# Kernel optimization log

Measured on AMD Instinct MI355X. Metric: run time of the kernel, lower is better.

Reference implementation:

```python
import jax, jax.numpy as jnp
import numpy as np

N, E = 100000, 1600000
NFEAT, NHID, NCLASS, NLAYER = 128, 128, 40, 3


def _glorot(key, shape):
    fan_in, fan_out = shape[0], shape[1]
    lim = float(np.sqrt(6.0 / (fan_in + fan_out)))
    return jax.random.uniform(key, shape, jnp.float32, -lim, lim)


def setup_inputs() -> dict:
    key = jax.random.key(0)
    ks = jax.random.split(key, 12)
    x = jax.random.normal(ks[0], (N, NFEAT), jnp.float32)
    src = jax.random.randint(ks[1], (E,), 0, N, jnp.int32)
    dst = jax.random.randint(ks[2], (E,), 0, N, jnp.int32)
    W1 = _glorot(ks[3], (NFEAT, NHID)); b1 = jnp.zeros((NHID,), jnp.float32)
    W2 = _glorot(ks[4], (NHID, NHID)); b2 = jnp.zeros((NHID,), jnp.float32)
    Wg = jnp.stack([_glorot(ks[5 + l], (NHID, NHID)) for l in range(NLAYER)])  # [L,H,H]
    bg = jnp.zeros((NLAYER, NHID), jnp.float32)
    Wc = _glorot(ks[5 + NLAYER], (NHID, NCLASS)); bc = jnp.zeros((NCLASS,), jnp.float32)
    return {"x": x, "src": src, "dst": dst, "W1": W1, "b1": b1, "W2": W2,
            "b2": b2, "Wg": Wg, "bg": bg, "Wc": Wc, "bc": bc}


def _graph_conv(h, src, dst, W, b, out_norm, in_norm):
    # DGL GraphConv norm='both': scale by src out-deg^{-1/2}, sum-aggregate,
    # scale by dst in-deg^{-1/2}, then linear (in_feats == out_feats -> W after agg).
    h = h * out_norm[:, None]
    agg = jax.ops.segment_sum(h[src], dst, num_segments=N)
    return (agg * in_norm[:, None]) @ W + b


def reference(x, src, dst, W1, b1, W2, b2, Wg, bg, Wc, bc):
    ones = jnp.ones((E,), jnp.float32)
    out_deg = jnp.clip(jax.ops.segment_sum(ones, src, num_segments=N), 1.0)
    in_deg = jnp.clip(jax.ops.segment_sum(ones, dst, num_segments=N), 1.0)
    out_norm = jax.lax.rsqrt(out_deg)
    in_norm = jax.lax.rsqrt(in_deg)

    h = x @ W1 + b1            # feature1
    h = h @ W2 + b2            # feature2
    for l in range(NLAYER):    # stacked GraphConv + ReLU (dropout is identity in eval)
        h = _graph_conv(h, src, dst, Wg[l], bg[l], out_norm, in_norm)
        h = jax.nn.relu(h)
    return h @ Wc + bc         # classifier
```

## Files before the change

### kernel.cpp

```cpp
#include <hip/hip_runtime.h>
#include <hip/hip_fp16.h>
#include <cstdint>
#include <cstddef>

constexpr int NN  = 100000;
constexpr int EE  = 1600000;
constexpr int HID = 128;
constexpr int BUK = 256;
constexpr int NBUK = (NN + BUK - 1) / BUK;
constexpr int BLKE = 2048;
constexpr int NBE  = (EE + BLKE - 1) / BLKE;
constexpr int MH   = NBUK * NBE;
constexpr int NSC  = (MH + 1023) / 1024;

typedef float f32x4_t __attribute__((ext_vector_type(4)));
typedef short bf16x8_t __attribute__((ext_vector_type(8)));

static __device__ __forceinline__ short f2bf(float f) {
    union { float f; unsigned u; } x; x.f = f;
    unsigned r = x.u + 0x7FFF + ((x.u >> 16) & 1);
    return (short)(r >> 16);
}
static __device__ __forceinline__ float bf2f(short b) {
    union { unsigned u; float f; } x; x.u = ((unsigned)(unsigned short)b) << 16;
    return x.f;
}

__global__ __launch_bounds__(256) void bh_both_k(const int* __restrict__ src, const int* __restrict__ dst,
                                                 int* __restrict__ bh_d, int* __restrict__ bh_s) {
    __shared__ int hd[NBUK], hs[NBUK];
    int blk = blockIdx.x, t = threadIdx.x;
    for (int i = t; i < NBUK; i += 256) { hd[i] = 0; hs[i] = 0; }
    __syncthreads();
    int e0 = blk * BLKE, e1 = min(e0 + BLKE, EE);
    for (int e = e0 + t; e < e1; e += 256) {
        atomicAdd(&hd[dst[e] >> 8], 1);
        atomicAdd(&hs[src[e] >> 8], 1);
    }
    __syncthreads();
    for (int i = t; i < NBUK; i += 256) {
        bh_d[i * NBE + blk] = hd[i];
        bh_s[i * NBE + blk] = hs[i];
    }
}

__global__ __launch_bounds__(256) void scan_sum_k(const int* __restrict__ in, int* __restrict__ bsum, int n) {
    __shared__ int sc[256];
    int b = blockIdx.x, t = threadIdx.x;
    int base = b * 1024 + t * 4;
    int s = 0;
#pragma unroll
    for (int j = 0; j < 4; j++) { int idx = base + j; s += (idx < n) ? in[idx] : 0; }
    sc[t] = s; __syncthreads();
    for (int off = 128; off > 0; off >>= 1) {
        if (t < off) sc[t] += sc[t + off];
        __syncthreads();
    }
    if (t == 0) bsum[b] = sc[0];
}

__global__ __launch_bounds__(512) void scan_top_k(const int* __restrict__ bsum, int* __restrict__ boff, int nb) {
    __shared__ int sc[512];
    int t = threadIdx.x;
    int v = (t < nb) ? bsum[t] : 0;
    sc[t] = v; __syncthreads();
    for (int off = 1; off < 512; off <<= 1) {
        int u = (t >= off) ? sc[t - off] : 0;
        __syncthreads();
        sc[t] += u;
        __syncthreads();
    }
    if (t < nb) boff[t] = sc[t] - v;
}

__global__ __launch_bounds__(256) void scan_chunk_k(const int* __restrict__ in, const int* __restrict__ boff,
                                                    int* __restrict__ out, int n) {
    __shared__ int sc[256];
    int b = blockIdx.x, t = threadIdx.x;
    int base = b * 1024 + t * 4;
    int c[4];
#pragma unroll
    for (int j = 0; j < 4; j++) { int idx = base + j; c[j] = (idx < n) ? in[idx] : 0; }
    int s = c[0] + c[1] + c[2] + c[3];
    sc[t] = s; __syncthreads();
    for (int off = 1; off < 256; off <<= 1) {
        int v = (t >= off) ? sc[t - off] : 0;
        __syncthreads();
        sc[t] += v;
        __syncthreads();
    }
    int excl = sc[t] - s + boff[b];
#pragma unroll
    for (int j = 0; j < 4; j++) {
        int idx = base + j;
        if (idx < n) out[idx] = excl;
        excl += c[j];
    }
}

__global__ __launch_bounds__(256) void scatter_both_k(const int* __restrict__ src, const int* __restrict__ dst,
                                                      const int* __restrict__ off_d, const int* __restrict__ off_s,
                                                      unsigned* __restrict__ pairs, unsigned char* __restrict__ sbyte) {
    __shared__ int cd[NBUK], cs[NBUK];
    int blk = blockIdx.x, t = threadIdx.x;
    for (int i = t; i < NBUK; i += 256) {
        cd[i] = off_d[i * NBE + blk];
        cs[i] = off_s[i * NBE + blk];
    }
    __syncthreads();
    int e0 = blk * BLKE, e1 = min(e0 + BLKE, EE);
    for (int e = e0 + t; e < e1; e += 256) {
        int d = dst[e], s = src[e];
        int pd = atomicAdd(&cd[d >> 8], 1);
        pairs[pd] = ((unsigned)(d & 255) << 17) | (unsigned)s;
        int ps = atomicAdd(&cs[s >> 8], 1);
        sbyte[ps] = (unsigned char)(s & 255);
    }
}

__global__ __launch_bounds__(512) void bucket_csr_ocnt_k(
    const unsigned* __restrict__ pairs, const int* __restrict__ off_d,
    const unsigned char* __restrict__ sbyte, const int* __restrict__ off_s,
    int* __restrict__ rowptr, int* __restrict__ col,
    float* __restrict__ inorm, float* __restrict__ onorm) {
    __shared__ int hist[BUK];
    __shared__ int excl[BUK];
    __shared__ int psum[BUK];
    int t = threadIdx.x;

    if (blockIdx.x >= NBUK) {
        int b = blockIdx.x - NBUK;
        int base = off_s[b * NBE];
        int endv = (b == NBUK - 1) ? EE : off_s[(b + 1) * NBE];
        if (t < BUK) hist[t] = 0;
        __syncthreads();
        for (int i = base + t; i < endv; i += 512) atomicAdd(&hist[sbyte[i]], 1);
        __syncthreads();
        if (t < BUK) {
            int node = b * BUK + t;
            if (node < NN) {
                int c = hist[t]; if (c < 1) c = 1;
                onorm[node] = rsqrtf((float)c);
            }
        }
        return;
    }

    int b = blockIdx.x;
    int base = off_d[b * NBE];
    int endv = (b == NBUK - 1) ? EE : off_d[(b + 1) * NBE];
    if (t < BUK) hist[t] = 0;
    __syncthreads();
    for (int i = base + t; i < endv; i += 512) atomicAdd(&hist[pairs[i] >> 17], 1);
    __syncthreads();
    int ps = 0;
    if (t < BUK) { ps = hist[t]; psum[t] = ps; }
    __syncthreads();
    for (int off = 1; off < BUK; off <<= 1) {
        int u = 0;
        if (t < BUK && t >= off) u = psum[t - off];
        __syncthreads();
        if (t < BUK) psum[t] += u;
        __syncthreads();
    }
    if (t < BUK) {
        int pex = psum[t] - ps;
        excl[t] = pex;
        int node = b * BUK + t;
        if (node < NN) {
            rowptr[node] = base + pex;
            int c = ps; if (c < 1) c = 1;
            inorm[node] = rsqrtf((float)c);
        }
    }
    if (b == NBUK - 1 && t == 0) rowptr[NN] = EE;
    __syncthreads();
    for (int i = base + t; i < endv; i += 512) {
        unsigned p = pairs[i];
        int pos = base + atomicAdd(&excl[p >> 17], 1);
        col[pos] = (int)(p & 0x1FFFFu);
    }
}

__global__ __launch_bounds__(256) void w12_k(const float* __restrict__ W1, const float* __restrict__ W2,
                                             const float* __restrict__ b1, const float* __restrict__ b2,
                                             float* __restrict__ W12, float* __restrict__ b12) {
    if (blockIdx.x == 64) {
        int j = threadIdx.x;
        if (j < 128) {
            float acc = b2[j];
            for (int k = 0; k < 128; k++) acc = fmaf(b1[k], W2[k * 128 + j], acc);
            b12[j] = acc;
        }
        return;
    }
    int idx = blockIdx.x * 256 + threadIdx.x;
    int i = idx >> 7, j = idx & 127;
    float a0 = 0.f, a1 = 0.f, a2 = 0.f, a3 = 0.f;
    for (int k = 0; k < 128; k += 4) {
        a0 = fmaf(W1[i * 128 + k],     W2[(k)     * 128 + j], a0);
        a1 = fmaf(W1[i * 128 + k + 1], W2[(k + 1) * 128 + j], a1);
        a2 = fmaf(W1[i * 128 + k + 2], W2[(k + 2) * 128 + j], a2);
        a3 = fmaf(W1[i * 128 + k + 3], W2[(k + 3) * 128 + j], a3);
    }
    W12[idx] = (a0 + a1) + (a2 + a3);
}

__global__ __launch_bounds__(256) void agg_k(const float4* __restrict__ h16, const int* __restrict__ rowptr,
                                             const int* __restrict__ col, float4* __restrict__ out) {
    int w = (int)((blockIdx.x * 256 + threadIdx.x) >> 6);
    if (w >= NN) return;
    int lane = threadIdx.x & 63;
    int q   = lane >> 4;
    int l16 = lane & 15;
    int beg = rowptr[w], end = rowptr[w + 1];
    float acc[8];
#pragma unroll
    for (int j = 0; j < 8; j++) acc[j] = 0.f;

    union HU { float4 f4; __half2 h2[4]; };
    int i = beg + q;
    for (; i + 12 < end; i += 16) {
        int s0 = col[i], s1 = col[i + 4], s2 = col[i + 8], s3 = col[i + 12];
        HU u0, u1, u2, u3;
        u0.f4 = h16[(size_t)s0 * 16 + l16];
        u1.f4 = h16[(size_t)s1 * 16 + l16];
        u2.f4 = h16[(size_t)s2 * 16 + l16];
        u3.f4 = h16[(size_t)s3 * 16 + l16];
#pragma unroll
        for (int p = 0; p < 4; p++) {
            float2 a = __half22float2(u0.h2[p]);
            float2 b = __half22float2(u1.h2[p]);
            float2 c = __half22float2(u2.h2[p]);
            float2 d = __half22float2(u3.h2[p]);
            acc[2 * p]     += (a.x + b.x) + (c.x + d.x);
            acc[2 * p + 1] += (a.y + b.y) + (c.y + d.y);
        }
    }
    for (; i < end; i += 4) {
        int s = col[i];
        HU u; u.f4 = h16[(size_t)s * 16 + l16];
#pragma unroll
        for (int p = 0; p < 4; p++) {
            float2 a = __half22float2(u.h2[p]);
            acc[2 * p]     += a.x;
            acc[2 * p + 1] += a.y;
        }
    }
#pragma unroll
    for (int mm = 16; mm <= 32; mm <<= 1)
#pragma unroll
        for (int j = 0; j < 8; j++) acc[j] += __shfl_xor(acc[j], mm);
    if (q == 0) {
        float4 o0, o1;
        o0.x = acc[0]; o0.y = acc[1]; o0.z = acc[2]; o0.w = acc[3];
        o1.x = acc[4]; o1.y = acc[5]; o1.z = acc[6]; o1.w = acc[7];
        out[(size_t)w * 32 + l16 * 2]     = o0;
        out[(size_t)w * 32 + l16 * 2 + 1] = o1;
    }
}

template <int NT, bool RELU, bool INSCALE, bool OUTSCALE, bool OUTHALF>
__global__ __launch_bounds__(256) void mfma_gemm_k(
    const float* __restrict__ in, const float* __restrict__ inscale,
    const float* __restrict__ W, const float* __restrict__ bias,
    void* __restrict__ outp, const float* __restrict__ outscale,
    int nrows, int ncols, int ntiles) {

    __shared__ short Bh[NT * 2048];
    __shared__ short Bl[NT * 2048];

    const int t = threadIdx.x;

    if constexpr (NT == 8) {
        for (int j = 0; j < 16; j++) {
            int fi = (j * 256 + t) * 4;
            int k = fi >> 7, n0 = fi & 127;
            float4 wv = *(const float4*)(W + fi);
            float wa[4] = {wv.x, wv.y, wv.z, wv.w};
#pragma unroll
            for (int cc = 0; cc < 4; cc++) {
                int g = n0 + cc;
                int q2 = g >> 2;
                int ntc = q2 & 7;
                int c = ((q2 >> 3) << 2) | (g & 3);
                int kblk = k >> 5, ksub = k & 31;
                int lane_ = ((ksub >> 3) << 4) | c;
                int sidx = ((ntc * 4 + kblk) * 64 + lane_) * 8 + (ksub & 7);
                short hi = f2bf(wa[cc]);
                Bh[sidx] = hi; Bl[sidx] = f2bf(wa[cc] - bf2f(hi));
            }
        }
    } else {
        for (int idx = t; idx < 128 * 64; idx += 256) {
            int k = idx >> 6, g = idx & 63;
            if (g < NT * 16) {
                float w = (g < 40) ? W[k * 40 + g] : 0.f;
                int q2 = g >> 2;
                int ntc = q2 % NT;
                int c = (q2 / NT) * 4 + (g & 3);
                int kblk = k >> 5, ksub = k & 31;
                int lane_ = ((ksub >> 3) << 4) | c;
                int sidx = ((ntc * 4 + kblk) * 64 + lane_) * 8 + (ksub & 7);
                short hi = f2bf(w);
                Bh[sidx] = hi; Bl[sidx] = f2bf(w - bf2f(hi));
            }
        }
    }
    __syncthreads();

    const int wave = t >> 6;
    const int lane = t & 63;
    const int m    = lane & 15;
    const int kq   = lane >> 4;
    const int cbase = kq * 4 * NT;

    float bstat[4 * NT];
#pragma unroll
    for (int i = 0; i < 4 * NT; i++) {
        int g = cbase + i;
        bstat[i] = (g < ncols) ? bias[g] : 0.f;
    }

    const int wstride = gridDim.x * 4;
    for (int tile = blockIdx.x * 4 + wave; tile < ntiles; tile += wstride) {
        int row = tile * 16 + m;
        bool rv = row < nrows;

        bf16x8_t Ah[4], Al[4];
        float s = 1.f;
        if (INSCALE && rv) s = inscale[row];
#pragma unroll
        for (int kb = 0; kb < 4; kb++) {
            const float* ap = in + (size_t)row * 128 + kb * 32 + kq * 8;
            float4 p0, p1;
            if (rv) { p0 = *(const float4*)ap; p1 = *(const float4*)(ap + 4); }
            else    { p0 = make_float4(0,0,0,0); p1 = make_float4(0,0,0,0); }
            float av[8] = {p0.x, p0.y, p0.z, p0.w, p1.x, p1.y, p1.z, p1.w};
#pragma unroll
            for (int j = 0; j < 8; j++) {
                float v = INSCALE ? av[j] * s : av[j];
                short hi = f2bf(v);
                Ah[kb][j] = hi;
                Al[kb][j] = f2bf(v - bf2f(hi));
            }
        }

        float osc = 1.f;
        if (OUTSCALE && rv) osc = outscale[row];

        float ov[4 * NT] __attribute__((aligned(16)));
#pragma unroll
        for (int nt = 0; nt < NT; nt++) {
            f32x4_t acc = {0.f, 0.f, 0.f, 0.f};
#pragma unroll
            for (int kb = 0; kb < 4; kb++) {
                const bf16x8_t bh = *(const bf16x8_t*)&Bh[((nt * 4 + kb) * 64 + lane) * 8];
                const bf16x8_t bl = *(const bf16x8_t*)&Bl[((nt * 4 + kb) * 64 + lane) * 8];
                acc = __builtin_amdgcn_mfma_f32_16x16x32_bf16(bh, Ah[kb], acc, 0, 0, 0);
                acc = __builtin_amdgcn_mfma_f32_16x16x32_bf16(bh, Al[kb], acc, 0, 0, 0);
                acc = __builtin_amdgcn_mfma_f32_16x16x32_bf16(bl, Ah[kb], acc, 0, 0, 0);
            }
#pragma unroll
            for (int r = 0; r < 4; r++) {
                float v = acc[r] + bstat[nt * 4 + r];
                if (RELU) v = fmaxf(v, 0.f);
                ov[nt * 4 + r] = v * osc;
            }
        }

        if (rv) {
            if constexpr (OUTHALF) {
                union { __half h[4 * NT]; float4 f4[NT]; } U;
#pragma unroll
                for (int i = 0; i < 4 * NT; i++) U.h[i] = __float2half_rn(ov[i]);
                float4* p = (float4*)((__half*)outp + (size_t)row * ncols + cbase);
#pragma unroll
                for (int j = 0; j < NT; j += 2) p[j >> 1] = U.f4[j >> 1];
            } else if constexpr (NT == 8) {
                float4* p = (float4*)((float*)outp + (size_t)row * 128 + cbase);
#pragma unroll
                for (int j = 0; j < 8; j++) p[j] = ((const float4*)ov)[j];
            } else {
                float* p = (float*)outp + (size_t)row * 40 + cbase;
#pragma unroll
                for (int j = 0; j < 3; j++) {
                    if (cbase + j * 4 < 40) *(float4*)(p + j * 4) = ((const float4*)ov)[j];
                }
            }
        }
    }
}

extern "C" void kernel_launch(void* const* d_in, const int* in_sizes, int n_in,
                              void* d_out, int out_size, void* d_ws, size_t ws_size,
                              hipStream_t stream) {
    const float* x   = (const float*)d_in[0];
    const int*   src = (const int*)d_in[1];
    const int*   dst = (const int*)d_in[2];
    const float* W1  = (const float*)d_in[3];
    const float* b1  = (const float*)d_in[4];
    const float* W2  = (const float*)d_in[5];
    const float* b2  = (const float*)d_in[6];
    const float* Wg  = (const float*)d_in[7];
    const float* bg  = (const float*)d_in[8];
    const float* Wc  = (const float*)d_in[9];
    const float* bc  = (const float*)d_in[10];
    float* out = (float*)d_out;

    char* ws = (char*)d_ws;
    size_t off = 0;
    auto alloc = [&](size_t bytes) -> void* {
        void* p = ws + off;
        off += (bytes + 255) & ~(size_t)255;
        return p;
    };
    float*  h0     = (float*)alloc((size_t)NN * HID * 4);
    float*  h1     = (float*)alloc((size_t)NN * HID * 4);
    __half* h16    = (__half*)alloc((size_t)NN * HID * 2);
    float*  W12    = (float*)alloc(128 * 128 * 4);
    float*  b12    = (float*)alloc(128 * 4);
    float*  onorm  = (float*)alloc((size_t)NN * 4);
    float*  inorm  = (float*)alloc((size_t)NN * 4);
    int*    rowptr = (int*)alloc((size_t)(NN + 1) * 4);
    int*    col    = (int*)alloc((size_t)EE * 4);
    int*    bh_d   = (int*)alloc((size_t)MH * 4);
    int*    bh_s   = (int*)alloc((size_t)MH * 4);
    int*    off_d  = (int*)alloc((size_t)MH * 4);
    int*    off_s  = (int*)alloc((size_t)MH * 4);
    int*    bsum   = (int*)alloc((size_t)NSC * 4);
    int*    boff   = (int*)alloc((size_t)NSC * 4);
    unsigned*      pairs = (unsigned*)h0;
    unsigned char* sbyte = (unsigned char*)h0 + (size_t)EE * 4;

    bh_both_k<<<NBE, 256, 0, stream>>>(src, dst, bh_d, bh_s);
    scan_sum_k<<<NSC, 256, 0, stream>>>(bh_d, bsum, MH);
    scan_top_k<<<1, 512, 0, stream>>>(bsum, boff, NSC);
    scan_chunk_k<<<NSC, 256, 0, stream>>>(bh_d, boff, off_d, MH);
    scan_sum_k<<<NSC, 256, 0, stream>>>(bh_s, bsum, MH);
    scan_top_k<<<1, 512, 0, stream>>>(bsum, boff, NSC);
    scan_chunk_k<<<NSC, 256, 0, stream>>>(bh_s, boff, off_s, MH);
    scatter_both_k<<<NBE, 256, 0, stream>>>(src, dst, off_d, off_s, pairs, sbyte);
    bucket_csr_ocnt_k<<<2 * NBUK, 512, 0, stream>>>(pairs, off_d, sbyte, off_s,
                                                    rowptr, col, inorm, onorm);

    w12_k<<<65, 256, 0, stream>>>(W1, W2, b1, b2, W12, b12);

    const int ntiles = (NN + 15) / 16;
    const int ggrid  = 512;

    mfma_gemm_k<8, false, false, true, true><<<ggrid, 256, 0, stream>>>(
        x, nullptr, W12, b12, h16, onorm, NN, 128, ntiles);
    for (int l = 0; l < 3; l++) {
        agg_k<<<(NN * 64 + 255) / 256, 256, 0, stream>>>(
            (const float4*)h16, rowptr, col, (float4*)h0);
        if (l < 2) {
            mfma_gemm_k<8, true, true, true, true><<<ggrid, 256, 0, stream>>>(
                h0, inorm, Wg + (size_t)l * 128 * 128, bg + (size_t)l * 128, h16, onorm, NN, 128, ntiles);
        } else {
            mfma_gemm_k<8, true, true, false, false><<<ggrid, 256, 0, stream>>>(
                h0, inorm, Wg + (size_t)l * 128 * 128, bg + (size_t)l * 128, h1, nullptr, NN, 128, ntiles);
        }
    }
    mfma_gemm_k<3, false, false, false, false><<<ggrid, 256, 0, stream>>>(
        h1, nullptr, Wc, bc, out, nullptr, NN, 40, ntiles);
}
```

Baseline: 558.6 us.

## Merge src/dst bucket scans, fold in-norm into aggregation, unroll agg tail

The dst and src bucket histograms now sit in one concatenated array, so a single three-kernel scan replaces two; src offsets are recovered by subtracting the edge count. The in-degree normalisation moves from the GEMM input path into the aggregation epilogue, and the aggregation tail loop handles two neighbours per iteration. This removes three small launches and a per-element scale in the GEMM load, and also changes ntiles to NN/16, which relies on NN being a multiple of 16.

```diff
diff --git a/kernel.cpp b/kernel.cpp
--- a/kernel.cpp
+++ b/kernel.cpp
@@ -11,7 +11,8 @@
 constexpr int BLKE = 2048;
 constexpr int NBE  = (EE + BLKE - 1) / BLKE;
 constexpr int MH   = NBUK * NBE;
-constexpr int NSC  = (MH + 1023) / 1024;
+constexpr int MH2  = 2 * MH;
+constexpr int NSC  = (MH2 + 2047) / 2048;
 
 typedef float f32x4_t __attribute__((ext_vector_type(4)));
 typedef short bf16x8_t __attribute__((ext_vector_type(8)));
@@ -27,7 +28,7 @@
 }
 
 __global__ __launch_bounds__(256) void bh_both_k(const int* __restrict__ src, const int* __restrict__ dst,
-                                                 int* __restrict__ bh_d, int* __restrict__ bh_s) {
+                                                 int* __restrict__ bh2) {
     __shared__ int hd[NBUK], hs[NBUK];
     int blk = blockIdx.x, t = threadIdx.x;
     for (int i = t; i < NBUK; i += 256) { hd[i] = 0; hs[i] = 0; }
@@ -39,18 +40,18 @@
     }
     __syncthreads();
     for (int i = t; i < NBUK; i += 256) {
-        bh_d[i * NBE + blk] = hd[i];
-        bh_s[i * NBE + blk] = hs[i];
+        bh2[i * NBE + blk]      = hd[i];
+        bh2[MH + i * NBE + blk] = hs[i];
     }
 }
 
 __global__ __launch_bounds__(256) void scan_sum_k(const int* __restrict__ in, int* __restrict__ bsum, int n) {
     __shared__ int sc[256];
     int b = blockIdx.x, t = threadIdx.x;
-    int base = b * 1024 + t * 4;
+    int base = b * 2048 + t * 8;
     int s = 0;
 #pragma unroll
-    for (int j = 0; j < 4; j++) { int idx = base + j; s += (idx < n) ? in[idx] : 0; }
+    for (int j = 0; j < 8; j++) { int idx = base + j; s += (idx < n) ? in[idx] : 0; }
     sc[t] = s; __syncthreads();
     for (int off = 128; off > 0; off >>= 1) {
         if (t < off) sc[t] += sc[t + off];
@@ -77,11 +78,11 @@
                                                     int* __restrict__ out, int n) {
     __shared__ int sc[256];
     int b = blockIdx.x, t = threadIdx.x;
-    int base = b * 1024 + t * 4;
-    int c[4];
-#pragma unroll
-    for (int j = 0; j < 4; j++) { int idx = base + j; c[j] = (idx < n) ? in[idx] : 0; }
-    int s = c[0] + c[1] + c[2] + c[3];
+    int base = b * 2048 + t * 8;
+    int c[8];
+    int s = 0;
+#pragma unroll
+    for (int j = 0; j < 8; j++) { int idx = base + j; c[j] = (idx < n) ? in[idx] : 0; s += c[j]; }
     sc[t] = s; __syncthreads();
     for (int off = 1; off < 256; off <<= 1) {
         int v = (t >= off) ? sc[t - off] : 0;
@@ -91,7 +92,7 @@
     }
     int excl = sc[t] - s + boff[b];
 #pragma unroll
-    for (int j = 0; j < 4; j++) {
+    for (int j = 0; j < 8; j++) {
         int idx = base + j;
         if (idx < n) out[idx] = excl;
         excl += c[j];
@@ -99,13 +100,13 @@
 }
 
 __global__ __launch_bounds__(256) void scatter_both_k(const int* __restrict__ src, const int* __restrict__ dst,
-                                                      const int* __restrict__ off_d, const int* __restrict__ off_s,
+                                                      const int* __restrict__ off2,
                                                       unsigned* __restrict__ pairs, unsigned char* __restrict__ sbyte) {
     __shared__ int cd[NBUK], cs[NBUK];
     int blk = blockIdx.x, t = threadIdx.x;
     for (int i = t; i < NBUK; i += 256) {
-        cd[i] = off_d[i * NBE + blk];
-        cs[i] = off_s[i * NBE + blk];
+        cd[i] = off2[i * NBE + blk];
+        cs[i] = off2[MH + i * NBE + blk] - EE;
     }
     __syncthreads();
     int e0 = blk * BLKE, e1 = min(e0 + BLKE, EE);
@@ -119,8 +120,8 @@
 }
 
 __global__ __launch_bounds__(512) void bucket_csr_ocnt_k(
-    const unsigned* __restrict__ pairs, const int* __restrict__ off_d,
-    const unsigned char* __restrict__ sbyte, const int* __restrict__ off_s,
+    const unsigned* __restrict__ pairs, const unsigned char* __restrict__ sbyte,
+    const int* __restrict__ off2,
     int* __restrict__ rowptr, int* __restrict__ col,
     float* __restrict__ inorm, float* __restrict__ onorm) {
     __shared__ int hist[BUK];
@@ -130,8 +131,8 @@
 
     if (blockIdx.x >= NBUK) {
         int b = blockIdx.x - NBUK;
-        int base = off_s[b * NBE];
-        int endv = (b == NBUK - 1) ? EE : off_s[(b + 1) * NBE];
+        int base = off2[MH + b * NBE] - EE;
+        int endv = (b == NBUK - 1) ? EE : off2[MH + (b + 1) * NBE] - EE;
         if (t < BUK) hist[t] = 0;
         __syncthreads();
         for (int i = base + t; i < endv; i += 512) atomicAdd(&hist[sbyte[i]], 1);
@@ -147,8 +148,8 @@
     }
 
     int b = blockIdx.x;
-    int base = off_d[b * NBE];
-    int endv = (b == NBUK - 1) ? EE : off_d[(b + 1) * NBE];
+    int base = off2[b * NBE];
+    int endv = (b == NBUK - 1) ? EE : off2[(b + 1) * NBE];
     if (t < BUK) hist[t] = 0;
     __syncthreads();
     for (int i = base + t; i < endv; i += 512) atomicAdd(&hist[pairs[i] >> 17], 1);
@@ -207,7 +208,8 @@
 }
 
 __global__ __launch_bounds__(256) void agg_k(const float4* __restrict__ h16, const int* __restrict__ rowptr,
-                                             const int* __restrict__ col, float4* __restrict__ out) {
+                                             const int* __restrict__ col, const float* __restrict__ inorm,
+                                             float4* __restrict__ out) {
     int w = (int)((blockIdx.x * 256 + threadIdx.x) >> 6);
     if (w >= NN) return;
     int lane = threadIdx.x & 63;
@@ -237,9 +239,21 @@
             acc[2 * p + 1] += (a.y + b.y) + (c.y + d.y);
         }
     }
-    for (; i < end; i += 4) {
-        int s = col[i];
-        HU u; u.f4 = h16[(size_t)s * 16 + l16];
+    for (; i + 4 < end; i += 8) {
+        int s0 = col[i], s1 = col[i + 4];
+        HU u0, u1;
+        u0.f4 = h16[(size_t)s0 * 16 + l16];
+        u1.f4 = h16[(size_t)s1 * 16 + l16];
+#pragma unroll
+        for (int p = 0; p < 4; p++) {
+            float2 a = __half22float2(u0.h2[p]);
+            float2 b = __half22float2(u1.h2[p]);
+            acc[2 * p]     += a.x + b.x;
+            acc[2 * p + 1] += a.y + b.y;
+        }
+    }
+    if (i < end) {
+        HU u; u.f4 = h16[(size_t)col[i] * 16 + l16];
 #pragma unroll
         for (int p = 0; p < 4; p++) {
             float2 a = __half22float2(u.h2[p]);
@@ -252,9 +266,10 @@
 #pragma unroll
         for (int j = 0; j < 8; j++) acc[j] += __shfl_xor(acc[j], mm);
     if (q == 0) {
+        float s = inorm[w];
         float4 o0, o1;
-        o0.x = acc[0]; o0.y = acc[1]; o0.z = acc[2]; o0.w = acc[3];
-        o1.x = acc[4]; o1.y = acc[5]; o1.z = acc[6]; o1.w = acc[7];
+        o0.x = acc[0] * s; o0.y = acc[1] * s; o0.z = acc[2] * s; o0.w = acc[3] * s;
+        o1.x = acc[4] * s; o1.y = acc[5] * s; o1.z = acc[6] * s; o1.w = acc[7] * s;
         out[(size_t)w * 32 + l16 * 2]     = o0;
         out[(size_t)w * 32 + l16 * 2 + 1] = o1;
     }
@@ -424,42 +439,37 @@
     float*  inorm  = (float*)alloc((size_t)NN * 4);
     int*    rowptr = (int*)alloc((size_t)(NN + 1) * 4);
     int*    col    = (int*)alloc((size_t)EE * 4);
-    int*    bh_d   = (int*)alloc((size_t)MH * 4);
-    int*    bh_s   = (int*)alloc((size_t)MH * 4);
-    int*    off_d  = (int*)alloc((size_t)MH * 4);
-    int*    off_s  = (int*)alloc((size_t)MH * 4);
+    int*    bh2    = (int*)alloc((size_t)MH2 * 4);
+    int*    off2   = (int*)alloc((size_t)MH2 * 4);
     int*    bsum   = (int*)alloc((size_t)NSC * 4);
     int*    boff   = (int*)alloc((size_t)NSC * 4);
     unsigned*      pairs = (unsigned*)h0;
     unsigned char* sbyte = (unsigned char*)h0 + (size_t)EE * 4;
 
-    bh_both_k<<<NBE, 256, 0, stream>>>(src, dst, bh_d, bh_s);
-    scan_sum_k<<<NSC, 256, 0, stream>>>(bh_d, bsum, MH);
+    bh_both_k<<<NBE, 256, 0, stream>>>(src, dst, bh2);
+    scan_sum_k<<<NSC, 256, 0, stream>>>(bh2, bsum, MH2);
     scan_top_k<<<1, 512, 0, stream>>>(bsum, boff, NSC);
-    scan_chunk_k<<<NSC, 256, 0, stream>>>(bh_d, boff, off_d, MH);
-    scan_sum_k<<<NSC, 256, 0, stream>>>(bh_s, bsum, MH);
-    scan_top_k<<<1, 512, 0, stream>>>(bsum, boff, NSC);
-    scan_chunk_k<<<NSC, 256, 0, stream>>>(bh_s, boff, off_s, MH);
-    scatter_both_k<<<NBE, 256, 0, stream>>>(src, dst, off_d, off_s, pairs, sbyte);
-    bucket_csr_ocnt_k<<<2 * NBUK, 512, 0, stream>>>(pairs, off_d, sbyte, off_s,
+    scan_chunk_k<<<NSC, 256, 0, stream>>>(bh2, boff, off2, MH2);
+    scatter_both_k<<<NBE, 256, 0, stream>>>(src, dst, off2, pairs, sbyte);
+    bucket_csr_ocnt_k<<<2 * NBUK, 512, 0, stream>>>(pairs, sbyte, off2,
                                                     rowptr, col, inorm, onorm);
 
     w12_k<<<65, 256, 0, stream>>>(W1, W2, b1, b2, W12, b12);
 
-    const int ntiles = (NN + 15) / 16;
+    const int ntiles = NN / 16;
     const int ggrid  = 512;
 
     mfma_gemm_k<8, false, false, true, true><<<ggrid, 256, 0, stream>>>(
         x, nullptr, W12, b12, h16, onorm, NN, 128, ntiles);
     for (int l = 0; l < 3; l++) {
         agg_k<<<(NN * 64 + 255) / 256, 256, 0, stream>>>(
-            (const float4*)h16, rowptr, col, (float4*)h0);
+            (const float4*)h16, rowptr, col, inorm, (float4*)h0);
         if (l < 2) {
-            mfma_gemm_k<8, true, true, true, true><<<ggrid, 256, 0, stream>>>(
-                h0, inorm, Wg + (size_t)l * 128 * 128, bg + (size_t)l * 128, h16, onorm, NN, 128, ntiles);
+            mfma_gemm_k<8, true, false, true, true><<<ggrid, 256, 0, stream>>>(
+                h0, nullptr, Wg + (size_t)l * 128 * 128, bg + (size_t)l * 128, h16, onorm, NN, 128, ntiles);
         } else {
-            mfma_gemm_k<8, true, true, false, false><<<ggrid, 256, 0, stream>>>(
-                h0, inorm, Wg + (size_t)l * 128 * 128, bg + (size_t)l * 128, h1, nullptr, NN, 128, ntiles);
+            mfma_gemm_k<8, true, false, false, false><<<ggrid, 256, 0, stream>>>(
+                h0, nullptr, Wg + (size_t)l * 128 * 128, bg + (size_t)l * 128, h1, nullptr, NN, 128, ntiles);
         }
     }
     mfma_gemm_k<3, false, false, false, false><<<ggrid, 256, 0, stream>>>(
```

After: 559.2 us. Within noise of the previous version (+0.1%).
